# Kernel tuning notes

Measured on AMD Instinct MI355X. Metric: run time of the kernel, lower is better.

Reference implementation:

```python
import jax, jax.numpy as jnp
import numpy as np

D_MODEL = 1024
N_HEADS = 16
HEAD_DIM = D_MODEL // N_HEADS
KV_LATENT = 512
N_EXPERTS = 4
D_HIDDEN = 4 * D_MODEL
B, T = 2, 1024


def rmsnorm(x, w, eps=1e-6):
    return w * (x * jax.lax.rsqrt(jnp.mean(x * x, axis=-1, keepdims=True) + eps))


def layernorm(x, g, b, eps=1e-5):
    mu = jnp.mean(x, axis=-1, keepdims=True)
    var = jnp.mean((x - mu) ** 2, axis=-1, keepdims=True)
    return (x - mu) * jax.lax.rsqrt(var + eps) * g + b


def apply_rope(x):
    # x: [b, h, t, d], half-split RoPE as in the torch source
    t, d = x.shape[2], x.shape[3]
    half = d // 2
    pos = jnp.arange(t, dtype=x.dtype)[:, None]                      # [t,1]
    inv_freq = 1.0 / (10000.0 ** (jnp.arange(half, dtype=x.dtype) / half))
    ang = pos * inv_freq[None, :]                                    # [t,half]
    sin, cos = jnp.sin(ang), jnp.cos(ang)
    x1, x2 = x[..., :half], x[..., half:]
    return jnp.concatenate([x1 * cos - x2 * sin, x1 * sin + x2 * cos], axis=-1)


def setup_inputs() -> dict:
    key = jax.random.key(0)
    ks = jax.random.split(key, 16)
    s = lambda fan_in: 1.0 / np.sqrt(fan_in)
    return {
        "x": jax.random.normal(ks[0], (B, T, D_MODEL), jnp.float32),
        "norm1_w": jnp.ones((D_MODEL,), jnp.float32),
        "norm2_w": jnp.ones((D_MODEL,), jnp.float32),
        "Wq": jax.random.normal(ks[1], (D_MODEL, D_MODEL), jnp.float32) * s(D_MODEL),
        "Wdkv": jax.random.normal(ks[2], (KV_LATENT, D_MODEL), jnp.float32) * s(D_MODEL),
        "Wuk": jax.random.normal(ks[3], (D_MODEL, KV_LATENT), jnp.float32) * s(KV_LATENT),
        "Wuv": jax.random.normal(ks[4], (D_MODEL, KV_LATENT), jnp.float32) * s(KV_LATENT),
        "Wo": jax.random.normal(ks[5], (D_MODEL, D_MODEL), jnp.float32) * s(D_MODEL),
        "ln_g": jnp.ones((KV_LATENT,), jnp.float32),
        "ln_b": jnp.zeros((KV_LATENT,), jnp.float32),
        "gate_w": jax.random.normal(ks[6], (N_EXPERTS, D_MODEL), jnp.float32) * s(D_MODEL),
        "gate_b": jnp.zeros((N_EXPERTS,), jnp.float32),
        "W1": jax.random.normal(ks[7], (N_EXPERTS, D_HIDDEN, D_MODEL), jnp.float32) * s(D_MODEL),
        "b1": jnp.zeros((N_EXPERTS, D_HIDDEN), jnp.float32),
        "W2": jax.random.normal(ks[8], (N_EXPERTS, D_MODEL, D_HIDDEN), jnp.float32) * s(D_HIDDEN),
        "b2": jnp.zeros((N_EXPERTS, D_MODEL), jnp.float32),
    }


def mla_attention(x, Wq, Wdkv, Wuk, Wuv, Wo, ln_g, ln_b):
    b, t, _ = x.shape
    q = (x @ Wq.T).reshape(b, t, N_HEADS, HEAD_DIM).transpose(0, 2, 1, 3)  # [b,h,t,dh]
    latent = layernorm(x @ Wdkv.T, ln_g, ln_b)                             # [b,t,L]
    k = (latent @ Wuk.T).reshape(b, t, N_HEADS, HEAD_DIM).transpose(0, 2, 1, 3)
    v = (latent @ Wuv.T).reshape(b, t, N_HEADS, HEAD_DIM).transpose(0, 2, 1, 3)
    q = apply_rope(q)
    k = apply_rope(k)
    scores = jnp.einsum("bhqd,bhkd->bhqk", q, k) / np.sqrt(HEAD_DIM)
    causal = jnp.tril(jnp.ones((t, t), dtype=bool))
    scores = jnp.where(causal, scores, -jnp.inf)
    attn = jax.nn.softmax(scores, axis=-1)  # dropout is identity in eval
    out = jnp.einsum("bhqk,bhkd->bhqd", attn, v).transpose(0, 2, 1, 3).reshape(b, t, D_MODEL)
    return out @ Wo.T


def moe(x, gate_w, gate_b, W1, b1, W2, b2):
    # top-1 routing: each token goes to exactly one expert (argmax of gate)
    logits = x @ gate_w.T + gate_b                                  # [b,t,E]
    top = jnp.argmax(logits, axis=-1)                               # [b,t]
    onehot = jax.nn.one_hot(top, N_EXPERTS, dtype=x.dtype)          # [b,t,E]
    h = jax.nn.relu(jnp.einsum("btd,ehd->bteh", x, W1) + b1)        # [b,t,E,H]
    y = jnp.einsum("bteh,edh->bted", h, W2) + b2                    # [b,t,E,D]
    return jnp.einsum("bted,bte->btd", y, onehot)


def reference(x, norm1_w, norm2_w, Wq, Wdkv, Wuk, Wuv, Wo, ln_g, ln_b,
              gate_w, gate_b, W1, b1, W2, b2):
    x = x + mla_attention(rmsnorm(x, norm1_w), Wq, Wdkv, Wuk, Wuv, Wo, ln_g, ln_b)
    x = x + moe(rmsnorm(x, norm2_w), gate_w, gate_b, W1, b1, W2, b2)
    return x
```

## Files before the change

### kernel.cpp

```cpp
#include <hip/hip_runtime.h>
#include <hip/hip_bf16.h>
#include <math.h>

typedef unsigned short u16;
typedef __attribute__((ext_vector_type(4))) float floatx4;
typedef __attribute__((ext_vector_type(8))) short shortx8;

#define DEVI static __device__ __forceinline__

DEVI u16 f2b(float f) {
  union { float f; unsigned int i; } v; v.f = f;
  unsigned int x = v.i;
  return (u16)((x + 0x7fffu + ((x >> 16) & 1u)) >> 16);
}

constexpr int T_ = 1024, D_ = 1024, HD_ = 64, KV_ = 512, DH_ = 4096, M_ = 2048;
#define NEGBIG (-1e30f)

__global__ __launch_bounds__(256) void k_rms1b(const float* __restrict__ x, const float* __restrict__ w,
                                               u16* __restrict__ outb) {
  int row = blockIdx.x, tid = threadIdx.x;
  float4 v = *(const float4*)&x[(size_t)row * D_ + tid * 4];
  float ss = v.x*v.x + v.y*v.y + v.z*v.z + v.w*v.w;
  #pragma unroll
  for (int m = 32; m >= 1; m >>= 1) ss += __shfl_xor(ss, m, 64);
  __shared__ float red[4];
  if ((tid & 63) == 0) red[tid >> 6] = ss;
  __syncthreads();
  ss = red[0] + red[1] + red[2] + red[3];
  float sc = 1.0f / sqrtf(ss * (1.0f / 1024.0f) + 1e-6f);
  float4 wv = *(const float4*)&w[tid * 4];
  ushort4 ob;
  ob.x = f2b(wv.x*v.x*sc); ob.y = f2b(wv.y*v.y*sc);
  ob.z = f2b(wv.z*v.z*sc); ob.w = f2b(wv.w*v.w*sc);
  *(ushort4*)&outb[(size_t)row * D_ + tid * 4] = ob;
}

__global__ __launch_bounds__(256) void k_rms2b(const float* __restrict__ x, const float* __restrict__ w,
                                               float* __restrict__ outf, u16* __restrict__ outb) {
  int row = blockIdx.x, tid = threadIdx.x;
  float4 v = *(const float4*)&x[(size_t)row * D_ + tid * 4];
  float ss = v.x*v.x + v.y*v.y + v.z*v.z + v.w*v.w;
  #pragma unroll
  for (int m = 32; m >= 1; m >>= 1) ss += __shfl_xor(ss, m, 64);
  __shared__ float red[4];
  if ((tid & 63) == 0) red[tid >> 6] = ss;
  __syncthreads();
  ss = red[0] + red[1] + red[2] + red[3];
  float sc = 1.0f / sqrtf(ss * (1.0f / 1024.0f) + 1e-6f);
  float4 wv = *(const float4*)&w[tid * 4];
  float4 o; o.x = wv.x*v.x*sc; o.y = wv.y*v.y*sc; o.z = wv.z*v.z*sc; o.w = wv.w*v.w*sc;
  *(float4*)&outf[(size_t)row * D_ + tid * 4] = o;
  ushort4 ob; ob.x = f2b(o.x); ob.y = f2b(o.y); ob.z = f2b(o.z); ob.w = f2b(o.w);
  *(ushort4*)&outb[(size_t)row * D_ + tid * 4] = ob;
}

__global__ __launch_bounds__(256) void k_lnb(const float* __restrict__ lat, const float* __restrict__ g,
                                             const float* __restrict__ bb, u16* __restrict__ ob) {
  int row = blockIdx.x, tid = threadIdx.x;
  const float* r = lat + (size_t)row * KV_;
  float v0 = r[tid], v1 = r[tid + 256];
  float s = v0 + v1;
  #pragma unroll
  for (int m = 32; m >= 1; m >>= 1) s += __shfl_xor(s, m, 64);
  __shared__ float red[4];
  if ((tid & 63) == 0) red[tid >> 6] = s;
  __syncthreads();
  float mu = (red[0] + red[1] + red[2] + red[3]) * (1.0f / 512.0f);
  __syncthreads();
  float d0 = v0 - mu, d1 = v1 - mu;
  float ss = d0*d0 + d1*d1;
  #pragma unroll
  for (int m = 32; m >= 1; m >>= 1) ss += __shfl_xor(ss, m, 64);
  if ((tid & 63) == 0) red[tid >> 6] = ss;
  __syncthreads();
  float var = (red[0] + red[1] + red[2] + red[3]) * (1.0f / 512.0f);
  float sc = 1.0f / sqrtf(var + 1e-5f);
  ob[(size_t)row * KV_ + tid]       = f2b(d0 * sc * g[tid]       + bb[tid]);
  ob[(size_t)row * KV_ + tid + 256] = f2b(d1 * sc * g[tid + 256] + bb[tid + 256]);
}

__global__ __launch_bounds__(256) void k_cvtall(const float* __restrict__ W1, const float* __restrict__ W2,
                                                const float* __restrict__ Wq, const float* __restrict__ Wdkv,
                                                const float* __restrict__ Wuk, const float* __restrict__ Wuv,
                                                const float* __restrict__ Wo, u16* __restrict__ dst) {
  for (size_t i = (size_t)blockIdx.x * 256 + threadIdx.x; i < 9306112ull; i += (size_t)gridDim.x * 256) {
    const float* s;
    if      (i < 4194304ull) s = W1   + i * 4;
    else if (i < 8388608ull) s = W2   + (i - 4194304ull) * 4;
    else if (i < 8650752ull) s = Wq   + (i - 8388608ull) * 4;
    else if (i < 8781824ull) s = Wdkv + (i - 8650752ull) * 4;
    else if (i < 8912896ull) s = Wuk  + (i - 8781824ull) * 4;
    else if (i < 9043968ull) s = Wuv  + (i - 8912896ull) * 4;
    else                     s = Wo   + (i - 9043968ull) * 4;
    float4 f = *(const float4*)s;
    ushort4 u; u.x = f2b(f.x); u.y = f2b(f.y); u.z = f2b(f.z); u.w = f2b(f.w);
    *(ushort4*)(dst + i * 4) = u;
  }
}

template<int BF16B>
__global__ __launch_bounds__(256) void k_gemm_t(const u16* __restrict__ A, const void* __restrict__ Bp,
                                                const float* __restrict__ resid, float* __restrict__ Cf,
                                                u16* __restrict__ Cb, int N, int K) {
  int bid = blockIdx.x;
  int xcd = bid & 7, jj = bid >> 3;
  int mt = jj & 31, nt = (jj >> 5) * 8 + xcd;
  __shared__ __align__(16) u16 As[64][72];
  __shared__ __align__(16) u16 Bs[64][72];
  int tid = threadIdx.x, lane = tid & 63, wave = tid >> 6;
  int wm = (wave >> 1) * 32, wn = (wave & 1) * 32;
  int lr = tid >> 2, lc = (tid & 3) * 16;
  const u16* arow = A + (size_t)(mt * 64 + lr) * K + lc;
  const u16* browb = (const u16*)Bp + (size_t)(nt * 64 + lr) * K + lc;
  const float* browf = (const float*)Bp + (size_t)(nt * 64 + lr) * K + lc;
  floatx4 z = {0.f, 0.f, 0.f, 0.f};
  floatx4 acc00 = z, acc01 = z, acc10 = z, acc11 = z;
  int fm = lane & 15, fkq = (lane >> 4) * 8;
  uint4 ra0 = *(const uint4*)&arow[0];
  uint4 ra1 = *(const uint4*)&arow[8];
  uint4 rbA, rbB; float4 rb0, rb1, rb2, rb3;
  if constexpr (BF16B) {
    rbA = *(const uint4*)&browb[0]; rbB = *(const uint4*)&browb[8];
  } else {
    rb0 = *(const float4*)&browf[0];  rb1 = *(const float4*)&browf[4];
    rb2 = *(const float4*)&browf[8];  rb3 = *(const float4*)&browf[12];
  }
  for (int kb = 0; kb < K; kb += 64) {
    *(uint4*)&As[lr][lc]     = ra0;
    *(uint4*)&As[lr][lc + 8] = ra1;
    if constexpr (BF16B) {
      *(uint4*)&Bs[lr][lc]     = rbA;
      *(uint4*)&Bs[lr][lc + 8] = rbB;
    } else {
      ushort4 u;
      u.x = f2b(rb0.x); u.y = f2b(rb0.y); u.z = f2b(rb0.z); u.w = f2b(rb0.w); *(ushort4*)&Bs[lr][lc]      = u;
      u.x = f2b(rb1.x); u.y = f2b(rb1.y); u.z = f2b(rb1.z); u.w = f2b(rb1.w); *(ushort4*)&Bs[lr][lc + 4]  = u;
      u.x = f2b(rb2.x); u.y = f2b(rb2.y); u.z = f2b(rb2.z); u.w = f2b(rb2.w); *(ushort4*)&Bs[lr][lc + 8]  = u;
      u.x = f2b(rb3.x); u.y = f2b(rb3.y); u.z = f2b(rb3.z); u.w = f2b(rb3.w); *(ushort4*)&Bs[lr][lc + 12] = u;
    }
    __syncthreads();
    if (kb + 64 < K) {
      ra0 = *(const uint4*)&arow[kb + 64];
      ra1 = *(const uint4*)&arow[kb + 72];
      if constexpr (BF16B) {
        rbA = *(const uint4*)&browb[kb + 64]; rbB = *(const uint4*)&browb[kb + 72];
      } else {
        rb0 = *(const float4*)&browf[kb + 64]; rb1 = *(const float4*)&browf[kb + 68];
        rb2 = *(const float4*)&browf[kb + 72]; rb3 = *(const float4*)&browf[kb + 76];
      }
    }
    #pragma unroll
    for (int ks = 0; ks < 64; ks += 32) {
      shortx8 a0  = *(const shortx8*)&As[wm + fm][ks + fkq];
      shortx8 a1  = *(const shortx8*)&As[wm + 16 + fm][ks + fkq];
      shortx8 b0  = *(const shortx8*)&Bs[wn + fm][ks + fkq];
      shortx8 b1v = *(const shortx8*)&Bs[wn + 16 + fm][ks + fkq];
      acc00 = __builtin_amdgcn_mfma_f32_16x16x32_bf16(a0, b0,  acc00, 0, 0, 0);
      acc01 = __builtin_amdgcn_mfma_f32_16x16x32_bf16(a0, b1v, acc01, 0, 0, 0);
      acc10 = __builtin_amdgcn_mfma_f32_16x16x32_bf16(a1, b0,  acc10, 0, 0, 0);
      acc11 = __builtin_amdgcn_mfma_f32_16x16x32_bf16(a1, b1v, acc11, 0, 0, 0);
    }
    __syncthreads();
  }
  int q4 = (lane >> 4) * 4, cix = lane & 15;
  #pragma unroll
  for (int im = 0; im < 2; ++im) {
    #pragma unroll
    for (int rg = 0; rg < 4; ++rg) {
      int row = mt * 64 + wm + im * 16 + q4 + rg;
      #pragma unroll
      for (int in = 0; in < 2; ++in) {
        int gn = nt * 64 + wn + in * 16 + cix;
        float vv = (im == 0 ? (in == 0 ? acc00[rg] : acc01[rg]) : (in == 0 ? acc10[rg] : acc11[rg]));
        size_t idx = (size_t)row * N + gn;
        if (Cb) {
          Cb[idx] = f2b(vv);
        } else {
          if (resid) vv += resid[idx];
          Cf[idx] = vv;
        }
      }
    }
  }
}

__global__ __launch_bounds__(256) void k_rope2b(const float* __restrict__ q, const float* __restrict__ k,
                                                u16* __restrict__ qb, u16* __restrict__ kb) {
  int g = blockIdx.x * 256 + threadIdx.x;
  int j = g & 31;
  int h = (g >> 5) & 15;
  int row = g >> 9;
  int t = row & (T_ - 1);
  float p = (float)pow(10000.0, (double)j * (1.0 / 32.0));
  float ang = (float)t / p;
  float sn, cs; sincosf(ang, &sn, &cs);
  size_t base = (size_t)row * D_ + h * 64 + j;
  float x1 = q[base], x2 = q[base + 32];
  qb[base]      = f2b((x1 * cs - x2 * sn) * 0.125f);
  qb[base + 32] = f2b((x1 * sn + x2 * cs) * 0.125f);
  x1 = k[base]; x2 = k[base + 32];
  kb[base]      = f2b(x1 * cs - x2 * sn);
  kb[base + 32] = f2b(x1 * sn + x2 * cs);
}

__global__ __launch_bounds__(256) void k_fattn(const u16* __restrict__ qbp, const u16* __restrict__ kbp,
                                               const u16* __restrict__ vbp, u16* __restrict__ ob) {
  int idx = blockIdx.x, h = blockIdx.y;
  int b = idx >> 4;
  int qt = idx & 15;
  if (b) qt = 15 - qt;
  __shared__ __align__(16) u16 Qs[64][72];
  __shared__ __align__(16) u16 Ks[64][72];
  __shared__ __align__(16) u16 Vs[64][72];
  __shared__ __align__(16) u16 Ps[64][72];
  int tid = threadIdx.x, lane = tid & 63, wave = tid >> 6;
  int fm = lane & 15, fkq = (lane >> 4) * 8;
  int q4 = (lane >> 4) * 4, cix = lane & 15;
  int w16 = wave * 16;
  size_t rowbase = (size_t)b * T_;
  int colbase = h * HD_;
  int q0 = qt * 64;
  int lr = tid >> 2, ld = (tid & 3) * 16;
  {
    const u16* qr = qbp + (rowbase + q0 + lr) * D_ + colbase + ld;
    *(uint4*)&Qs[lr][ld]     = *(const uint4*)&qr[0];
    *(uint4*)&Qs[lr][ld + 8] = *(const uint4*)&qr[8];
  }
  floatx4 z = {0.f, 0.f, 0.f, 0.f};
  floatx4 s[4], o[4];
  o[0] = z; o[1] = z; o[2] = z; o[3] = z;
  float m[4], l[4];
  #pragma unroll
  for (int rg = 0; rg < 4; ++rg) { m[rg] = NEGBIG; l[rg] = 0.f; }
  const u16* kr = kbp + (rowbase + lr) * D_ + colbase + ld;
  const u16* vr = vbp + (rowbase + lr) * D_ + colbase + ld;
  uint4 rk0 = *(const uint4*)&kr[0], rk1 = *(const uint4*)&kr[8];
  uint4 rv0 = *(const uint4*)&vr[0], rv1 = *(const uint4*)&vr[8];
  for (int kt = 0; kt <= qt; ++kt) {
    __syncthreads();
    *(uint4*)&Ks[lr][ld]     = rk0;
    *(uint4*)&Ks[lr][ld + 8] = rk1;
    {
      union { uint4 v4[2]; u16 e[16]; } vv;
      vv.v4[0] = rv0; vv.v4[1] = rv1;
      #pragma unroll
      for (int c = 0; c < 16; ++c) Vs[ld + c][lr] = vv.e[c];
    }
    __syncthreads();
    if (kt < qt) {
      kr += 64 * D_; vr += 64 * D_;
      rk0 = *(const uint4*)&kr[0]; rk1 = *(const uint4*)&kr[8];
      rv0 = *(const uint4*)&vr[0]; rv1 = *(const uint4*)&vr[8];
    }
    s[0] = z; s[1] = z; s[2] = z; s[3] = z;
    #pragma unroll
    for (int ks = 0; ks < 64; ks += 32) {
      shortx8 a = *(const shortx8*)&Qs[w16 + fm][ks + fkq];
      #pragma unroll
      for (int nb = 0; nb < 4; ++nb) {
        shortx8 bb = *(const shortx8*)&Ks[nb * 16 + fm][ks + fkq];
        s[nb] = __builtin_amdgcn_mfma_f32_16x16x32_bf16(a, bb, s[nb], 0, 0, 0);
      }
    }
    if (kt == qt) {
      #pragma unroll
      for (int nb = 0; nb < 4; ++nb)
        #pragma unroll
        for (int rg = 0; rg < 4; ++rg)
          if (nb * 16 + cix > w16 + q4 + rg) s[nb][rg] = NEGBIG;
    }
    #pragma unroll
    for (int rg = 0; rg < 4; ++rg) {
      float mx = fmaxf(fmaxf(s[0][rg], s[1][rg]), fmaxf(s[2][rg], s[3][rg]));
      #pragma unroll
      for (int mk = 8; mk >= 1; mk >>= 1) mx = fmaxf(mx, __shfl_xor(mx, mk, 64));
      float mn = fmaxf(m[rg], mx);
      float f = __expf(m[rg] - mn);
      m[rg] = mn;
      float p0 = __expf(s[0][rg] - mn);
      float p1 = __expf(s[1][rg] - mn);
      float p2 = __expf(s[2][rg] - mn);
      float p3 = __expf(s[3][rg] - mn);
      float rs = (p0 + p1) + (p2 + p3);
      #pragma unroll
      for (int mk = 8; mk >= 1; mk >>= 1) rs += __shfl_xor(rs, mk, 64);
      l[rg] = l[rg] * f + rs;
      o[0][rg] *= f; o[1][rg] *= f; o[2][rg] *= f; o[3][rg] *= f;
      int prow = w16 + q4 + rg;
      Ps[prow][cix]      = f2b(p0);
      Ps[prow][16 + cix] = f2b(p1);
      Ps[prow][32 + cix] = f2b(p2);
      Ps[prow][48 + cix] = f2b(p3);
    }
    #pragma unroll
    for (int ks = 0; ks < 64; ks += 32) {
      shortx8 a = *(const shortx8*)&Ps[w16 + fm][ks + fkq];
      #pragma unroll
      for (int db = 0; db < 4; ++db) {
        shortx8 bb = *(const shortx8*)&Vs[db * 16 + fm][ks + fkq];
        o[db] = __builtin_amdgcn_mfma_f32_16x16x32_bf16(a, bb, o[db], 0, 0, 0);
      }
    }
  }
  #pragma unroll
  for (int rg = 0; rg < 4; ++rg) {
    float inv = 1.0f / l[rg];
    size_t base = (rowbase + q0 + w16 + q4 + rg) * D_ + colbase;
    #pragma unroll
    for (int db = 0; db < 4; ++db)
      ob[base + db * 16 + cix] = f2b(o[db][rg] * inv);
  }
}

__global__ __launch_bounds__(256) void k_init(int* cnt) { if (threadIdx.x < 4) cnt[threadIdx.x] = 0; }

__global__ __launch_bounds__(256) void k_gate(const float* __restrict__ h2, const float* __restrict__ gw,
                                              const float* __restrict__ gb, int* __restrict__ expert,
                                              int* __restrict__ cnt) {
  int wid = threadIdx.x >> 6, lane = threadIdx.x & 63;
  int t = blockIdx.x * 4 + wid;
  const float* hr = h2 + (size_t)t * D_;
  float a0 = 0, a1 = 0, a2 = 0, a3 = 0;
  for (int c = lane; c < D_; c += 64) {
    float xv = hr[c];
    a0 += xv * gw[c];
    a1 += xv * gw[D_ + c];
    a2 += xv * gw[2 * D_ + c];
    a3 += xv * gw[3 * D_ + c];
  }
  #pragma unroll
  for (int m = 32; m >= 1; m >>= 1) {
    a0 += __shfl_xor(a0, m, 64); a1 += __shfl_xor(a1, m, 64);
    a2 += __shfl_xor(a2, m, 64); a3 += __shfl_xor(a3, m, 64);
  }
  if (lane == 0) {
    float l0 = a0 + gb[0], l1 = a1 + gb[1], l2 = a2 + gb[2], l3 = a3 + gb[3];
    int best = 0; float bv = l0;
    if (l1 > bv) { bv = l1; best = 1; }
    if (l2 > bv) { bv = l2; best = 2; }
    if (l3 > bv) { bv = l3; best = 3; }
    expert[t] = best;
    atomicAdd(&cnt[best], 1);
  }
}

__global__ __launch_bounds__(256) void k_scatter(const int* __restrict__ expert, const int* __restrict__ cnt,
                                                 int* __restrict__ off, int* __restrict__ sorted) {
  __shared__ int cur[4];
  if (threadIdx.x == 0) {
    int o0 = 0, o1 = cnt[0], o2 = o1 + cnt[1], o3 = o2 + cnt[2];
    off[0] = o0; off[1] = o1; off[2] = o2; off[3] = o3;
    cur[0] = o0; cur[1] = o1; cur[2] = o2; cur[3] = o3;
  }
  __syncthreads();
  for (int t = threadIdx.x; t < M_; t += 256) {
    int e = expert[t];
    int p = atomicAdd(&cur[e], 1);
    sorted[p] = t;
  }
}

template<int BF16B>
__global__ __launch_bounds__(256) void k_moe1_t(const u16* __restrict__ A, const void* __restrict__ W1p,
                                                const float* __restrict__ b1, const int* __restrict__ cnt,
                                                const int* __restrict__ off, const int* __restrict__ sorted,
                                                u16* __restrict__ hbuf) {
  int bid = blockIdx.x;
  int xcd = bid & 7, jj = bid >> 3;
  int mt = jj & 31, combo = (jj >> 5) * 8 + xcd;
  int e = combo >> 6, nt = combo & 63;
  int rem = cnt[e] - mt * 64;
  if (rem <= 0) return;
  __shared__ __align__(16) u16 As[64][72];
  __shared__ __align__(16) u16 Bs[64][72];
  int tid = threadIdx.x, lane = tid & 63, wave = tid >> 6;
  int wm = (wave >> 1) * 32, wn = (wave & 1) * 32;
  int lr = tid >> 2, lc = (tid & 3) * 16;
  int rr = lr < rem ? lr : rem - 1;
  const u16* arow = A + (size_t)sorted[off[e] + mt * 64 + rr] * D_ + lc;
  const u16* browb = (const u16*)W1p + (size_t)e * DH_ * D_ + (size_t)(nt * 64 + lr) * D_ + lc;
  const float* browf = (const float*)W1p + (size_t)e * DH_ * D_ + (size_t)(nt * 64 + lr) * D_ + lc;
  floatx4 z = {0.f, 0.f, 0.f, 0.f};
  floatx4 acc00 = z, acc01 = z, acc10 = z, acc11 = z;
  int fm = lane & 15, fkq = (lane >> 4) * 8;
  uint4 ra0 = *(const uint4*)&arow[0];
  uint4 ra1 = *(const uint4*)&arow[8];
  uint4 rbA, rbB; float4 rb0, rb1, rb2, rb3;
  if constexpr (BF16B) {
    rbA = *(const uint4*)&browb[0]; rbB = *(const uint4*)&browb[8];
  } else {
    rb0 = *(const float4*)&browf[0];  rb1 = *(const float4*)&browf[4];
    rb2 = *(const float4*)&browf[8];  rb3 = *(const float4*)&browf[12];
  }
  for (int kb = 0; kb < D_; kb += 64) {
    *(uint4*)&As[lr][lc]     = ra0;
    *(uint4*)&As[lr][lc + 8] = ra1;
    if constexpr (BF16B) {
      *(uint4*)&Bs[lr][lc]     = rbA;
      *(uint4*)&Bs[lr][lc + 8] = rbB;
    } else {
      ushort4 u;
      u.x = f2b(rb0.x); u.y = f2b(rb0.y); u.z = f2b(rb0.z); u.w = f2b(rb0.w); *(ushort4*)&Bs[lr][lc]      = u;
      u.x = f2b(rb1.x); u.y = f2b(rb1.y); u.z = f2b(rb1.z); u.w = f2b(rb1.w); *(ushort4*)&Bs[lr][lc + 4]  = u;
      u.x = f2b(rb2.x); u.y = f2b(rb2.y); u.z = f2b(rb2.z); u.w = f2b(rb2.w); *(ushort4*)&Bs[lr][lc + 8]  = u;
      u.x = f2b(rb3.x); u.y = f2b(rb3.y); u.z = f2b(rb3.z); u.w = f2b(rb3.w); *(ushort4*)&Bs[lr][lc + 12] = u;
    }
    __syncthreads();
    if (kb + 64 < D_) {
      ra0 = *(const uint4*)&arow[kb + 64];
      ra1 = *(const uint4*)&arow[kb + 72];
      if constexpr (BF16B) {
        rbA = *(const uint4*)&browb[kb + 64]; rbB = *(const uint4*)&browb[kb + 72];
      } else {
        rb0 = *(const float4*)&browf[kb + 64]; rb1 = *(const float4*)&browf[kb + 68];
        rb2 = *(const float4*)&browf[kb + 72]; rb3 = *(const float4*)&browf[kb + 76];
      }
    }
    #pragma unroll
    for (int ks = 0; ks < 64; ks += 32) {
      shortx8 a0  = *(const shortx8*)&As[wm + fm][ks + fkq];
      shortx8 a1  = *(const shortx8*)&As[wm + 16 + fm][ks + fkq];
      shortx8 b0  = *(const shortx8*)&Bs[wn + fm][ks + fkq];
      shortx8 b1v = *(const shortx8*)&Bs[wn + 16 + fm][ks + fkq];
      acc00 = __builtin_amdgcn_mfma_f32_16x16x32_bf16(a0, b0,  acc00, 0, 0, 0);
      acc01 = __builtin_amdgcn_mfma_f32_16x16x32_bf16(a0, b1v, acc01, 0, 0, 0);
      acc10 = __builtin_amdgcn_mfma_f32_16x16x32_bf16(a1, b0,  acc10, 0, 0, 0);
      acc11 = __builtin_amdgcn_mfma_f32_16x16x32_bf16(a1, b1v, acc11, 0, 0, 0);
    }
    __syncthreads();
  }
  int q4 = (lane >> 4) * 4, cix = lane & 15;
  #pragma unroll
  for (int im = 0; im < 2; ++im) {
    #pragma unroll
    for (int rg = 0; rg < 4; ++rg) {
      int ml = wm + im * 16 + q4 + rg;
      if (ml >= rem) continue;
      size_t grow = (size_t)(off[e] + mt * 64 + ml);
      #pragma unroll
      for (int in = 0; in < 2; ++in) {
        int gn = nt * 64 + wn + in * 16 + cix;
        float vv = (im == 0 ? (in == 0 ? acc00[rg] : acc01[rg]) : (in == 0 ? acc10[rg] : acc11[rg]));
        vv += b1[e * DH_ + gn];
        hbuf[grow * DH_ + gn] = f2b(fmaxf(vv, 0.f));
      }
    }
  }
}

template<int BF16B>
__global__ __launch_bounds__(256) void k_moe2_t(const u16* __restrict__ hbuf, const void* __restrict__ W2p,
                                                const float* __restrict__ b2w, const float* __restrict__ x1f,
                                                const int* __restrict__ cnt, const int* __restrict__ off,
                                                const int* __restrict__ sorted, float* __restrict__ out) {
  int bid = blockIdx.x;
  int xcd = bid & 7, jj = bid >> 3;
  int mt = jj & 31, combo = (jj >> 5) * 8 + xcd;
  int e = combo >> 4, nt = combo & 15;
  int rem = cnt[e] - mt * 64;
  if (rem <= 0) return;
  __shared__ __align__(16) u16 As[64][72];
  __shared__ __align__(16) u16 Bs[64][72];
  int tid = threadIdx.x, lane = tid & 63, wave = tid >> 6;
  int wm = (wave >> 1) * 32, wn = (wave & 1) * 32;
  int lr = tid >> 2, lc = (tid & 3) * 16;
  int rr = lr < rem ? lr : rem - 1;
  const u16* arow = hbuf + (size_t)(off[e] + mt * 64 + rr) * DH_ + lc;
  const u16* browb = (const u16*)W2p + (size_t)e * D_ * DH_ + (size_t)(nt * 64 + lr) * DH_ + lc;
  const float* browf = (const float*)W2p + (size_t)e * D_ * DH_ + (size_t)(nt * 64 + lr) * DH_ + lc;
  floatx4 z = {0.f, 0.f, 0.f, 0.f};
  floatx4 acc00 = z, acc01 = z, acc10 = z, acc11 = z;
  int fm = lane & 15, fkq = (lane >> 4) * 8;
  uint4 ra0 = *(const uint4*)&arow[0];
  uint4 ra1 = *(const uint4*)&arow[8];
  uint4 rbA, rbB; float4 rb0, rb1, rb2, rb3;
  if constexpr (BF16B) {
    rbA = *(const uint4*)&browb[0]; rbB = *(const uint4*)&browb[8];
  } else {
    rb0 = *(const float4*)&browf[0];  rb1 = *(const float4*)&browf[4];
    rb2 = *(const float4*)&browf[8];  rb3 = *(const float4*)&browf[12];
  }
  for (int kb = 0; kb < DH_; kb += 64) {
    *(uint4*)&As[lr][lc]     = ra0;
    *(uint4*)&As[lr][lc + 8] = ra1;
    if constexpr (BF16B) {
      *(uint4*)&Bs[lr][lc]     = rbA;
      *(uint4*)&Bs[lr][lc + 8] = rbB;
    } else {
      ushort4 u;
      u.x = f2b(rb0.x); u.y = f2b(rb0.y); u.z = f2b(rb0.z); u.w = f2b(rb0.w); *(ushort4*)&Bs[lr][lc]      = u;
      u.x = f2b(rb1.x); u.y = f2b(rb1.y); u.z = f2b(rb1.z); u.w = f2b(rb1.w); *(ushort4*)&Bs[lr][lc + 4]  = u;
      u.x = f2b(rb2.x); u.y = f2b(rb2.y); u.z = f2b(rb2.z); u.w = f2b(rb2.w); *(ushort4*)&Bs[lr][lc + 8]  = u;
      u.x = f2b(rb3.x); u.y = f2b(rb3.y); u.z = f2b(rb3.z); u.w = f2b(rb3.w); *(ushort4*)&Bs[lr][lc + 12] = u;
    }
    __syncthreads();
    if (kb + 64 < DH_) {
      ra0 = *(const uint4*)&arow[kb + 64];
      ra1 = *(const uint4*)&arow[kb + 72];
      if constexpr (BF16B) {
        rbA = *(const uint4*)&browb[kb + 64]; rbB = *(const uint4*)&browb[kb + 72];
      } else {
        rb0 = *(const float4*)&browf[kb + 64]; rb1 = *(const float4*)&browf[kb + 68];
        rb2 = *(const float4*)&browf[kb + 72]; rb3 = *(const float4*)&browf[kb + 76];
      }
    }
    #pragma unroll
    for (int ks = 0; ks < 64; ks += 32) {
      shortx8 a0  = *(const shortx8*)&As[wm + fm][ks + fkq];
      shortx8 a1  = *(const shortx8*)&As[wm + 16 + fm][ks + fkq];
      shortx8 b0  = *(const shortx8*)&Bs[wn + fm][ks + fkq];
      shortx8 b1v = *(const shortx8*)&Bs[wn + 16 + fm][ks + fkq];
      acc00 = __builtin_amdgcn_mfma_f32_16x16x32_bf16(a0, b0,  acc00, 0, 0, 0);
      acc01 = __builtin_amdgcn_mfma_f32_16x16x32_bf16(a0, b1v, acc01, 0, 0, 0);
      acc10 = __builtin_amdgcn_mfma_f32_16x16x32_bf16(a1, b0,  acc10, 0, 0, 0);
      acc11 = __builtin_amdgcn_mfma_f32_16x16x32_bf16(a1, b1v, acc11, 0, 0, 0);
    }
    __syncthreads();
  }
  int q4 = (lane >> 4) * 4, cix = lane & 15;
  #pragma unroll
  for (int im = 0; im < 2; ++im) {
    #pragma unroll
    for (int rg = 0; rg < 4; ++rg) {
      int ml = wm + im * 16 + q4 + rg;
      if (ml >= rem) continue;
      int tok = sorted[off[e] + mt * 64 + ml];
      #pragma unroll
      for (int in = 0; in < 2; ++in) {
        int gn = nt * 64 + wn + in * 16 + cix;
        float vv = (im == 0 ? (in == 0 ? acc00[rg] : acc01[rg]) : (in == 0 ? acc10[rg] : acc11[rg]));
        out[(size_t)tok * D_ + gn] = vv + b2w[e * D_ + gn] + x1f[(size_t)tok * D_ + gn];
      }
    }
  }
}

__global__ __launch_bounds__(256) void k_moe2s(const u16* __restrict__ hbuf, const u16* __restrict__ W2b,
                                               const int* __restrict__ cnt, const int* __restrict__ off,
                                               float* __restrict__ pbuf) {
  int bid = blockIdx.x;
  int xcd = bid & 7, jj = bid >> 3;
  int mt = jj & 31;
  int combo = (jj >> 5) * 8 + xcd;
  int ks = combo & 1, ec = combo >> 1;
  int e = ec >> 4, nt = ec & 15;
  int rem = cnt[e] - mt * 64;
  if (rem <= 0) return;
  const int KS = DH_ / 2;
  int k0 = ks * KS;
  __shared__ __align__(16) u16 As[64][72];
  __shared__ __align__(16) u16 Bs[64][72];
  int tid = threadIdx.x, lane = tid & 63, wave = tid >> 6;
  int wm = (wave >> 1) * 32, wn = (wave & 1) * 32;
  int lr = tid >> 2, lc = (tid & 3) * 16;
  int rr = lr < rem ? lr : rem - 1;
  const u16* arow = hbuf + (size_t)(off[e] + mt * 64 + rr) * DH_ + k0 + lc;
  const u16* brow = W2b + (size_t)e * D_ * DH_ + (size_t)(nt * 64 + lr) * DH_ + k0 + lc;
  floatx4 z = {0.f, 0.f, 0.f, 0.f};
  floatx4 acc00 = z, acc01 = z, acc10 = z, acc11 = z;
  int fm = lane & 15, fkq = (lane >> 4) * 8;
  uint4 ra0 = *(const uint4*)&arow[0];
  uint4 ra1 = *(const uint4*)&arow[8];
  uint4 rbA = *(const uint4*)&brow[0];
  uint4 rbB = *(const uint4*)&brow[8];
  for (int kb = 0; kb < KS; kb += 64) {
    *(uint4*)&As[lr][lc]     = ra0;
    *(uint4*)&As[lr][lc + 8] = ra1;
    *(uint4*)&Bs[lr][lc]     = rbA;
    *(uint4*)&Bs[lr][lc + 8] = rbB;
    __syncthreads();
    if (kb + 64 < KS) {
      ra0 = *(const uint4*)&arow[kb + 64];
      ra1 = *(const uint4*)&arow[kb + 72];
      rbA = *(const uint4*)&brow[kb + 64];
      rbB = *(const uint4*)&brow[kb + 72];
    }
    #pragma unroll
    for (int kk = 0; kk < 64; kk += 32) {
      shortx8 a0  = *(const shortx8*)&As[wm + fm][kk + fkq];
      shortx8 a1  = *(const shortx8*)&As[wm + 16 + fm][kk + fkq];
      shortx8 b0  = *(const shortx8*)&Bs[wn + fm][kk + fkq];
      shortx8 b1v = *(const shortx8*)&Bs[wn + 16 + fm][kk + fkq];
      acc00 = __builtin_amdgcn_mfma_f32_16x16x32_bf16(a0, b0,  acc00, 0, 0, 0);
      acc01 = __builtin_amdgcn_mfma_f32_16x16x32_bf16(a0, b1v, acc01, 0, 0, 0);
      acc10 = __builtin_amdgcn_mfma_f32_16x16x32_bf16(a1, b0,  acc10, 0, 0, 0);
      acc11 = __builtin_amdgcn_mfma_f32_16x16x32_bf16(a1, b1v, acc11, 0, 0, 0);
    }
    __syncthreads();
  }
  float* pb = pbuf + (size_t)ks * M_ * D_;
  int q4 = (lane >> 4) * 4, cix = lane & 15;
  #pragma unroll
  for (int im = 0; im < 2; ++im) {
    #pragma unroll
    for (int rg = 0; rg < 4; ++rg) {
      int ml = wm + im * 16 + q4 + rg;
      if (ml >= rem) continue;
      size_t srow = (size_t)(off[e] + mt * 64 + ml);
      #pragma unroll
      for (int in = 0; in < 2; ++in) {
        int gn = nt * 64 + wn + in * 16 + cix;
        float vv = (im == 0 ? (in == 0 ? acc00[rg] : acc01[rg]) : (in == 0 ? acc10[rg] : acc11[rg]));
        pb[srow * D_ + gn] = vv;
      }
    }
  }
}

__global__ __launch_bounds__(256) void k_moered(const float* __restrict__ pbuf, const float* __restrict__ b2w,
                                                const float* __restrict__ x1f, const int* __restrict__ off,
                                                const int* __restrict__ sorted, float* __restrict__ out) {
  int r = blockIdx.x, tid = threadIdx.x;
  int tok = sorted[r];
  int e = (r >= off[3]) ? 3 : (r >= off[2]) ? 2 : (r >= off[1]) ? 1 : 0;
  size_t c = (size_t)tid * 4;
  float4 a = *(const float4*)&pbuf[(size_t)r * D_ + c];
  float4 b = *(const float4*)&pbuf[(size_t)M_ * D_ + (size_t)r * D_ + c];
  float4 bb = *(const float4*)&b2w[(size_t)e * D_ + c];
  float4 xr = *(const float4*)&x1f[(size_t)tok * D_ + c];
  float4 o;
  o.x = a.x + b.x + bb.x + xr.x;
  o.y = a.y + b.y + bb.y + xr.y;
  o.z = a.z + b.z + bb.z + xr.z;
  o.w = a.w + b.w + bb.w + xr.w;
  *(float4*)&out[(size_t)tok * D_ + c] = o;
}

extern "C" void kernel_launch(void* const* d_in, const int* in_sizes, int n_in,
                              void* d_out, int out_size, void* d_ws, size_t ws_size,
                              hipStream_t stream) {
  int map[16];
  for (int i = 0; i < 16; ++i) map[i] = i;
  if (n_in == 16 && in_sizes[0] == 16777216) {
    const int mm[16] = {15, 13, 14, 4, 2, 5, 6, 3, 12, 11, 10, 9, 0, 7, 1, 8};
    for (int i = 0; i < 16; ++i) map[i] = mm[i];
  } else if (n_in == 16 && in_sizes[0] == 4096) {
    for (int i = 0; i < 16; ++i) map[i] = 15 - i;
  }
  const float* x    = (const float*)d_in[map[0]];
  const float* n1w  = (const float*)d_in[map[1]];
  const float* n2w  = (const float*)d_in[map[2]];
  const float* Wq   = (const float*)d_in[map[3]];
  const float* Wdkv = (const float*)d_in[map[4]];
  const float* Wuk  = (const float*)d_in[map[5]];
  const float* Wuv  = (const float*)d_in[map[6]];
  const float* Wo   = (const float*)d_in[map[7]];
  const float* lng  = (const float*)d_in[map[8]];
  const float* lnb  = (const float*)d_in[map[9]];
  const float* gw   = (const float*)d_in[map[10]];
  const float* gb   = (const float*)d_in[map[11]];
  const float* W1   = (const float*)d_in[map[12]];
  const float* b1   = (const float*)d_in[map[13]];
  const float* W2   = (const float*)d_in[map[14]];
  const float* b2w  = (const float*)d_in[map[15]];
  float* out = (float*)d_out;
  char* ws = (char*)d_ws;
  const size_t MB = 1ull << 20;
  float* qf   = (float*)(ws + 0);
  float* x1f  = (float*)(ws + 0);
  float* kf   = (float*)(ws + 8 * MB);
  u16*   hbuf = (u16*)(ws + 8 * MB);
  float* latf = (float*)(ws + 16 * MB);
  u16*   qb   = (u16*)(ws + 16 * MB);
  u16*   h1b  = (u16*)(ws + 20 * MB);
  u16*   kb   = (u16*)(ws + 20 * MB);
  u16*   latb = (u16*)(ws + 24 * MB);
  float* h2f  = (float*)(ws + 24 * MB);
  u16*   vb   = (u16*)(ws + 26 * MB);
  u16*   ab   = (u16*)(ws + 30 * MB);
  u16*   h2b  = (u16*)(ws + 32 * MB);
  float* pbuf = (float*)(ws + 24 * MB);

  bool big = ws_size >= (107ull * MB + (64ull << 10));
  u16* wb = (u16*)(ws + 36 * MB);
  u16* W1b   = wb;
  u16* W2b   = wb + 16777216;
  u16* Wqb   = wb + 33554432;
  u16* Wdkvb = wb + 34603008;
  u16* Wukb  = wb + 35127296;
  u16* Wuvb  = wb + 35651584;
  u16* Wob   = wb + 36175872;
  int* cnt    = (int*)(ws + (big ? 107 * MB : 36 * MB));
  int* off    = cnt + 8;
  int* expert = cnt + 16;
  int* sorted = expert + 2048;

  if (big) {
    k_cvtall<<<2048, 256, 0, stream>>>(W1, W2, Wq, Wdkv, Wuk, Wuv, Wo, wb);
    k_rms1b<<<2048, 256, 0, stream>>>(x, n1w, h1b);
    k_gemm_t<1><<<512, 256, 0, stream>>>(h1b, Wqb, nullptr, qf, nullptr, 1024, 1024);
    k_gemm_t<1><<<256, 256, 0, stream>>>(h1b, Wdkvb, nullptr, latf, nullptr, 512, 1024);
    k_lnb<<<2048, 256, 0, stream>>>(latf, lng, lnb, latb);
    k_gemm_t<1><<<512, 256, 0, stream>>>(latb, Wukb, nullptr, kf, nullptr, 1024, 512);
    k_gemm_t<1><<<512, 256, 0, stream>>>(latb, Wuvb, nullptr, nullptr, vb, 1024, 512);
    k_rope2b<<<4096, 256, 0, stream>>>(qf, kf, qb, kb);
    k_fattn<<<dim3(32, 16), 256, 0, stream>>>(qb, kb, vb, ab);
    k_gemm_t<1><<<512, 256, 0, stream>>>(ab, Wob, x, x1f, nullptr, 1024, 1024);
    k_rms2b<<<2048, 256, 0, stream>>>(x1f, n2w, h2f, h2b);
    k_init<<<1, 64, 0, stream>>>(cnt);
    k_gate<<<512, 256, 0, stream>>>(h2f, gw, gb, expert, cnt);
    k_scatter<<<1, 256, 0, stream>>>(expert, cnt, off, sorted);
    k_moe1_t<1><<<8192, 256, 0, stream>>>(h2b, W1b, b1, cnt, off, sorted, hbuf);
    k_moe2s<<<4096, 256, 0, stream>>>(hbuf, W2b, cnt, off, pbuf);
    k_moered<<<2048, 256, 0, stream>>>(pbuf, b2w, x1f, off, sorted, out);
  } else {
    k_rms1b<<<2048, 256, 0, stream>>>(x, n1w, h1b);
    k_gemm_t<0><<<512, 256, 0, stream>>>(h1b, Wq, nullptr, qf, nullptr, 1024, 1024);
    k_gemm_t<0><<<256, 256, 0, stream>>>(h1b, Wdkv, nullptr, latf, nullptr, 512, 1024);
    k_lnb<<<2048, 256, 0, stream>>>(latf, lng, lnb, latb);
    k_gemm_t<0><<<512, 256, 0, stream>>>(latb, Wuk, nullptr, kf, nullptr, 1024, 512);
    k_gemm_t<0><<<512, 256, 0, stream>>>(latb, Wuv, nullptr, nullptr, vb, 1024, 512);
    k_rope2b<<<4096, 256, 0, stream>>>(qf, kf, qb, kb);
    k_fattn<<<dim3(32, 16), 256, 0, stream>>>(qb, kb, vb, ab);
    k_gemm_t<0><<<512, 256, 0, stream>>>(ab, Wo, x, x1f, nullptr, 1024, 1024);
    k_rms2b<<<2048, 256, 0, stream>>>(x1f, n2w, h2f, h2b);
    k_init<<<1, 64, 0, stream>>>(cnt);
    k_gate<<<512, 256, 0, stream>>>(h2f, gw, gb, expert, cnt);
    k_scatter<<<1, 256, 0, stream>>>(expert, cnt, off, sorted);
    k_moe1_t<0><<<8192, 256, 0, stream>>>(h2b, W1, b1, cnt, off, sorted, hbuf);
    k_moe2_t<0><<<2048, 256, 0, stream>>>(hbuf, W2, b2w, x1f, cnt, off, sorted, out);
  }
}
```

Before: 436.8 us.

## Overlap MoE weight bf16 conversion with flash attention via extra blocks

The fp32-to-bf16 conversion of the large expert weights W1/W2 moves out of the upfront conversion kernel and into extra blocks appended to the flash-attention launch. The small attention weights are still converted first. The attention grid is flattened to 1D and blocks past 512 do the conversion, so memory-bound conversion can run alongside compute-bound attention. The risk is that conversion blocks compete for CUs and bandwidth with attention blocks, or get scheduled late and stretch the attention kernel.

```diff
diff --git a/kernel.cpp b/kernel.cpp
--- a/kernel.cpp
+++ b/kernel.cpp
@@ -80,15 +80,13 @@
   ob[(size_t)row * KV_ + tid + 256] = f2b(d1 * sc * g[tid + 256] + bb[tid + 256]);
 }
 
-__global__ __launch_bounds__(256) void k_cvtall(const float* __restrict__ W1, const float* __restrict__ W2,
-                                                const float* __restrict__ Wq, const float* __restrict__ Wdkv,
-                                                const float* __restrict__ Wuk, const float* __restrict__ Wuv,
-                                                const float* __restrict__ Wo, u16* __restrict__ dst) {
-  for (size_t i = (size_t)blockIdx.x * 256 + threadIdx.x; i < 9306112ull; i += (size_t)gridDim.x * 256) {
+__global__ __launch_bounds__(256) void k_cvt_small(const float* __restrict__ Wq, const float* __restrict__ Wdkv,
+                                                   const float* __restrict__ Wuk, const float* __restrict__ Wuv,
+                                                   const float* __restrict__ Wo, u16* __restrict__ dst) {
+  for (size_t i = 8388608ull + (size_t)blockIdx.x * 256 + threadIdx.x; i < 9306112ull;
+       i += (size_t)gridDim.x * 256) {
     const float* s;
-    if      (i < 4194304ull) s = W1   + i * 4;
-    else if (i < 8388608ull) s = W2   + (i - 4194304ull) * 4;
-    else if (i < 8650752ull) s = Wq   + (i - 8388608ull) * 4;
+    if      (i < 8650752ull) s = Wq   + (i - 8388608ull) * 4;
     else if (i < 8781824ull) s = Wdkv + (i - 8650752ull) * 4;
     else if (i < 8912896ull) s = Wuk  + (i - 8781824ull) * 4;
     else if (i < 9043968ull) s = Wuv  + (i - 8912896ull) * 4;
@@ -205,8 +203,22 @@
 }
 
 __global__ __launch_bounds__(256) void k_fattn(const u16* __restrict__ qbp, const u16* __restrict__ kbp,
-                                               const u16* __restrict__ vbp, u16* __restrict__ ob) {
-  int idx = blockIdx.x, h = blockIdx.y;
+                                               const u16* __restrict__ vbp, u16* __restrict__ ob,
+                                               const float* __restrict__ W1c, const float* __restrict__ W2c,
+                                               u16* __restrict__ wdst, int ncvt) {
+  int gid = blockIdx.x;
+  if (gid >= 512) {
+    size_t start = (size_t)(gid - 512) * 256 + threadIdx.x;
+    size_t stride = (size_t)ncvt * 256;
+    for (size_t i = start; i < 8388608ull; i += stride) {
+      const float* s = (i < 4194304ull) ? W1c + i * 4 : W2c + (i - 4194304ull) * 4;
+      float4 f = *(const float4*)s;
+      ushort4 u; u.x = f2b(f.x); u.y = f2b(f.y); u.z = f2b(f.z); u.w = f2b(f.w);
+      *(ushort4*)(wdst + i * 4) = u;
+    }
+    return;
+  }
+  int idx = gid & 31, h = gid >> 5;
   int b = idx >> 4;
   int qt = idx & 15;
   if (b) qt = 15 - qt;
@@ -687,7 +699,7 @@
   int* sorted = expert + 2048;
 
   if (big) {
-    k_cvtall<<<2048, 256, 0, stream>>>(W1, W2, Wq, Wdkv, Wuk, Wuv, Wo, wb);
+    k_cvt_small<<<1024, 256, 0, stream>>>(Wq, Wdkv, Wuk, Wuv, Wo, wb);
     k_rms1b<<<2048, 256, 0, stream>>>(x, n1w, h1b);
     k_gemm_t<1><<<512, 256, 0, stream>>>(h1b, Wqb, nullptr, qf, nullptr, 1024, 1024);
     k_gemm_t<1><<<256, 256, 0, stream>>>(h1b, Wdkvb, nullptr, latf, nullptr, 512, 1024);
@@ -695,7 +707,7 @@
     k_gemm_t<1><<<512, 256, 0, stream>>>(latb, Wukb, nullptr, kf, nullptr, 1024, 512);
     k_gemm_t<1><<<512, 256, 0, stream>>>(latb, Wuvb, nullptr, nullptr, vb, 1024, 512);
     k_rope2b<<<4096, 256, 0, stream>>>(qf, kf, qb, kb);
-    k_fattn<<<dim3(32, 16), 256, 0, stream>>>(qb, kb, vb, ab);
+    k_fattn<<<1024, 256, 0, stream>>>(qb, kb, vb, ab, W1, W2, wb, 512);
     k_gemm_t<1><<<512, 256, 0, stream>>>(ab, Wob, x, x1f, nullptr, 1024, 1024);
     k_rms2b<<<2048, 256, 0, stream>>>(x1f, n2w, h2f, h2b);
     k_init<<<1, 64, 0, stream>>>(cnt);
@@ -712,7 +724,7 @@
     k_gemm_t<0><<<512, 256, 0, stream>>>(latb, Wuk, nullptr, kf, nullptr, 1024, 512);
     k_gemm_t<0><<<512, 256, 0, stream>>>(latb, Wuv, nullptr, nullptr, vb, 1024, 512);
     k_rope2b<<<4096, 256, 0, stream>>>(qf, kf, qb, kb);
-    k_fattn<<<dim3(32, 16), 256, 0, stream>>>(qb, kb, vb, ab);
+    k_fattn<<<512, 256, 0, stream>>>(qb, kb, vb, ab, nullptr, nullptr, nullptr, 0);
     k_gemm_t<0><<<512, 256, 0, stream>>>(ab, Wo, x, x1f, nullptr, 1024, 1024);
     k_rms2b<<<2048, 256, 0, stream>>>(x1f, n2w, h2f, h2b);
     k_init<<<1, 64, 0, stream>>>(cnt);
```

New measurement: 416.8 us. -4.6%, faster.
